# Kernel optimization log

Measured on AMD Instinct MI355X. Metric: run time of the kernel, lower is better.

Reference implementation:

```python
import jax, jax.numpy as jnp
import numpy as np

B, C, H, W = 8, 512, 128, 128
WS = 8

def _proj(x, w, b):
    # 1x1 conv == channel GEMM: (B,C,H,W) x (Cout,Cin) -> (B,Cout,H,W)
    return jnp.einsum('bchw,oc->bohw', x, w) + b[None, :, None, None]

def _split_windows(x):
    # (B,C,H,W) -> (B*nH*nW, ws*ws, C)
    b, c, h, w = x.shape
    x = x.reshape(b, c, h // WS, WS, w // WS, WS)
    x = x.transpose(0, 2, 4, 3, 5, 1)
    return x.reshape(-1, WS * WS, c)

def _merge_windows(x, b, c, h, w):
    # (B*nH*nW, ws*ws, C) -> (B,C,H,W)
    x = x.reshape(b, h // WS, w // WS, WS, WS, c)
    x = x.transpose(0, 5, 1, 3, 2, 4)
    return x.reshape(b, c, h, w)

def setup_inputs() -> dict:
    key = jax.random.key(0)
    ks = jax.random.split(key, 9)
    s = 1.0 / np.sqrt(C)
    return {
        'x': jax.random.normal(ks[0], (B, C, H, W), jnp.float32),
        'wq': jax.random.normal(ks[1], (C, C), jnp.float32) * s,
        'bq': jnp.zeros((C,), jnp.float32),
        'wk': jax.random.normal(ks[2], (C, C), jnp.float32) * s,
        'bk': jnp.zeros((C,), jnp.float32),
        'wv': jax.random.normal(ks[3], (C, C), jnp.float32) * s,
        'bv': jnp.zeros((C,), jnp.float32),
        'wo': jax.random.normal(ks[4], (C, C), jnp.float32) * s,
        'bo': jnp.zeros((C,), jnp.float32),
    }

def reference(x, wq, bq, wk, bk, wv, bv, wo, bo):
    b, c, h, w = x.shape
    q = _split_windows(_proj(x, wq, bq))  # (nWin, ws*ws, C)
    k = _split_windows(_proj(x, wk, bk))
    v = _split_windows(_proj(x, wv, bv))
    attn = jnp.einsum('nqc,nkc->nqk', q, k) / jnp.sqrt(jnp.asarray(c, x.dtype))
    attn = jax.nn.softmax(attn, axis=-1)
    out = jnp.einsum('nqk,nkc->nqc', attn, v)
    out = _merge_windows(out, b, c, h, w)
    return _proj(out, wo, bo)
```

## Files before the change

### kernel.cpp

```cpp
#include <hip/hip_runtime.h>

typedef __attribute__((ext_vector_type(8))) short bf16x8;
typedef __attribute__((ext_vector_type(4))) float f32x4;

#define MFMA16(a, b, c) __builtin_amdgcn_mfma_f32_16x16x32_bf16((a), (b), (c), 0, 0, 0)

__device__ __forceinline__ float b2f(unsigned short u) {
  unsigned int v = ((unsigned int)u) << 16;
  return __builtin_bit_cast(float, v);
}
__device__ __forceinline__ unsigned short f2b(float f) {
  unsigned int u = __builtin_bit_cast(unsigned int, f);
  u += 0x7fffu + ((u >> 16) & 1u);
  return (unsigned short)(u >> 16);
}
__device__ __forceinline__ void gload16(const void* g, void* l) {
  __builtin_amdgcn_global_load_lds(
      (const __attribute__((address_space(1))) unsigned int*)g,
      (__attribute__((address_space(3))) unsigned int*)l, 16, 0, 0);
}

__global__ __launch_bounds__(256) void k_wprep(
    const float* __restrict__ wq, const float* __restrict__ wk,
    const float* __restrict__ wv, const float* __restrict__ wo,
    unsigned short* __restrict__ outbase) {
  const int z = blockIdx.z;
  const int t = threadIdx.x;
  if (z == 3) {
    const int r0 = blockIdx.x << 6, s0 = blockIdx.y << 6;
    const int row = r0 + (t >> 2), col = s0 + (t & 3) * 16;
    const float* src = wo + (size_t)row * 512 + col;
    unsigned short* dst = outbase + 786432 + (size_t)row * 512 + col;
    unsigned short o[16];
#pragma unroll
    for (int i = 0; i < 4; ++i) {
      const float4 v = ((const float4*)src)[i];
      o[i * 4 + 0] = f2b(v.x); o[i * 4 + 1] = f2b(v.y);
      o[i * 4 + 2] = f2b(v.z); o[i * 4 + 3] = f2b(v.w);
    }
    *(uint4*)dst = *(const uint4*)&o[0];
    *(uint4*)(dst + 8) = *(const uint4*)&o[8];
    return;
  }
  __shared__ unsigned short tile[64][72];
  const float* in = (z == 0) ? wq : (z == 1) ? wk : wv;
  unsigned short* out = outbase + (size_t)z * 262144u;
  const int r0 = blockIdx.x << 6, s0 = blockIdx.y << 6;
  {
    const int sl = t >> 3, rl = (t & 7) << 3;
#pragma unroll
    for (int pass = 0; pass < 2; ++pass) {
      const int s = sl + pass * 32;
      const float* src = in + (size_t)(s0 + s) * 512 + r0 + rl;
      const float4 f0 = ((const float4*)src)[0];
      const float4 f1 = ((const float4*)src)[1];
      tile[rl + 0][s] = f2b(f0.x);
      tile[rl + 1][s] = f2b(f0.y);
      tile[rl + 2][s] = f2b(f0.z);
      tile[rl + 3][s] = f2b(f0.w);
      tile[rl + 4][s] = f2b(f1.x);
      tile[rl + 5][s] = f2b(f1.y);
      tile[rl + 6][s] = f2b(f1.z);
      tile[rl + 7][s] = f2b(f1.w);
    }
  }
  __syncthreads();
  {
    const int rl = t >> 3, sl = (t & 7) << 3;
#pragma unroll
    for (int pass = 0; pass < 2; ++pass) {
      const int r = rl + pass * 32;
      uint4 v = *(const uint4*)&tile[r][sl];
      *(uint4*)(out + (size_t)(r0 + r) * 512 + s0 + sl) = v;
    }
  }
}

__global__ __launch_bounds__(256) void k_bias(
    const float* __restrict__ wo, const float* __restrict__ bv,
    const float* __restrict__ bo, const float* __restrict__ wk,
    const float* __restrict__ bq, float* __restrict__ bvo,
    float* __restrict__ u) {
  const int bid = blockIdx.x;
  if (bid < 2) {
    const int o = bid * 256 + threadIdx.x;
    float acc = bo[o];
    const float* row = wo + (size_t)o * 512;
    for (int j = 0; j < 512; ++j) acc += row[j] * bv[j];
    bvo[o] = acc;
  } else {
    const int c = (bid - 2) * 256 + threadIdx.x;
    float acc = 0.f;
    for (int o = 0; o < 512; ++o) acc += bq[o] * wk[(size_t)o * 512 + c];
    u[c] = acc;
  }
}

__global__ __launch_bounds__(256, 2) void k_transpose(
    const float* __restrict__ X, unsigned short* __restrict__ XT,
    unsigned short* __restrict__ XV) {
  __shared__ float lds[2][16 * 512];
  const int hz = blockIdx.x;
  const int cg = blockIdx.y;
  const int b = blockIdx.z;
  const int h0 = hz << 2;
  const int c0 = cg << 7;
  const int t = threadIdx.x;
  const float* xb = X + (size_t)b * 8388608u + (size_t)c0 * 16384 +
                    (size_t)h0 * 128;

  auto stage = [&](int s) {
    float* dstb = lds[s & 1];
#pragma unroll
    for (int i = 0; i < 8; ++i) {
      const int cl = i * 2 + (t >> 7);
      const int q = (i * 256 + t) & 127;
      gload16(xb + (size_t)(s * 16 + cl) * 16384 + q * 4,
              dstb + (size_t)(i * 256 + t) * 4);
    }
  };

  auto consume = [&](int s) {
    const float* L = lds[s & 1];
#pragma unroll
    for (int pp = 0; pp < 2; ++pp) {
      const int p = t + pp * 256;
      unsigned short o[16];
#pragma unroll
      for (int cl = 0; cl < 16; ++cl) o[cl] = f2b(L[cl * 512 + p]);
      unsigned short* d =
          XT + ((size_t)b * 16384 + h0 * 128 + p) * 512 + c0 + s * 16;
      *(uint4*)d = *(const uint4*)&o[0];
      *(uint4*)(d + 8) = *(const uint4*)&o[8];
    }
    {
      const int cl = t >> 4, win = t & 15;
      unsigned short ov[32];
#pragma unroll
      for (int hr = 0; hr < 4; ++hr) {
        const float4 f0 = *(const float4*)&L[cl * 512 + hr * 128 + win * 8];
        const float4 f1 = *(const float4*)&L[cl * 512 + hr * 128 + win * 8 + 4];
        ov[hr * 8 + 0] = f2b(f0.x); ov[hr * 8 + 1] = f2b(f0.y);
        ov[hr * 8 + 2] = f2b(f0.z); ov[hr * 8 + 3] = f2b(f0.w);
        ov[hr * 8 + 4] = f2b(f1.x); ov[hr * 8 + 5] = f2b(f1.y);
        ov[hr * 8 + 6] = f2b(f1.z); ov[hr * 8 + 7] = f2b(f1.w);
      }
      const int wing = b * 256 + (h0 >> 3) * 16 + win;
      const int tok0 = (h0 & 4) * 8;
      unsigned short* dv = XV + (size_t)(c0 + s * 16 + cl) * 131072 +
                           (size_t)wing * 64 + tok0;
      *(uint4*)(dv + 0) = *(const uint4*)&ov[0];
      *(uint4*)(dv + 8) = *(const uint4*)&ov[8];
      *(uint4*)(dv + 16) = *(const uint4*)&ov[16];
      *(uint4*)(dv + 24) = *(const uint4*)&ov[24];
    }
  };

  stage(0);
#pragma unroll
  for (int s = 0; s < 8; ++s) {
    if (s < 7) {
      stage(s + 1);
      asm volatile("s_waitcnt vmcnt(8)" ::: "memory");
    } else {
      asm volatile("s_waitcnt vmcnt(0)" ::: "memory");
    }
    __builtin_amdgcn_s_barrier();
    consume(s);
    __builtin_amdgcn_s_barrier();
  }
}

template <int MODE>
__global__ __launch_bounds__(512, 2) void k_gemm256(
    const unsigned short* __restrict__ A, const unsigned short* __restrict__ B,
    const float* __restrict__ bias0, void* __restrict__ C0v) {
  __shared__ unsigned short lsA[4][256 * 32];
  __shared__ unsigned short lsB[4][256 * 32];
  const int bid = blockIdx.x;
  int mt, nt, sel = 0;
  if (MODE == 0) {
    const int work = ((bid & 7) << 7) + (bid >> 3);
    mt = work >> 1; nt = work & 1;
  } else if (MODE == 2) {
    const int work = ((bid & 7) << 7) + (bid >> 3);
    nt = work >> 1; mt = work & 1;
  } else {
    sel = bid >> 2;
    mt = bid & 1; nt = (bid >> 1) & 1;
  }
  const unsigned short* Ap = A;
  const unsigned short* Bp = B;
  if (MODE == 4) {
    Ap = sel ? A + 786432 : A + 262144;
    Bp = sel ? A + 524288 : A;
  }
  const int m0 = mt << 8, n0 = nt << 8;

  const int t = threadIdx.x;
  const int l = t & 63;
  const int lr = l & 15, lg = l >> 4;
  const int w = t >> 6;
  const int wr = w >> 2, wc = w & 3;
  const int ra = wr << 7, rb = wc << 6;
  const int srowS = t >> 2;
  const int scolS = (t & 3) << 3;
  const int ssw = ((srowS >> 1) & 3) << 3;
  const int scolX = scolS ^ ssw;
  const int rsw = (lr >> 1) & 3;
  const int rco = (lg ^ rsw) * 8;

  f32x4 acc[8][4];
#pragma unroll
  for (int i = 0; i < 8; ++i)
#pragma unroll
    for (int j = 0; j < 4; ++j) acc[i][j] = f32x4{0.f, 0.f, 0.f, 0.f};

  auto stage = [&](int kt) {
    const int buf = kt & 3, k0 = kt << 5;
#pragma unroll
    for (int hh = 0; hh < 2; ++hh) {
      gload16(Ap + (size_t)(m0 + srowS + hh * 128) * 512 + k0 + scolX,
              &lsA[buf][(srowS + hh * 128) * 32 + scolS]);
      gload16(Bp + (size_t)(n0 + srowS + hh * 128) * 512 + k0 + scolX,
              &lsB[buf][(srowS + hh * 128) * 32 + scolS]);
    }
  };
  auto compute = [&](int kt) {
    const int buf = kt & 3;
    bf16x8 af[8], bfv[4];
#pragma unroll
    for (int i = 0; i < 8; ++i)
      af[i] = *(const bf16x8*)&lsA[buf][(ra + i * 16 + lr) * 32 + rco];
#pragma unroll
    for (int j = 0; j < 4; ++j)
      bfv[j] = *(const bf16x8*)&lsB[buf][(rb + j * 16 + lr) * 32 + rco];
    __builtin_amdgcn_s_setprio(1);
#pragma unroll
    for (int i = 0; i < 8; ++i)
#pragma unroll
      for (int j = 0; j < 4; ++j)
        acc[i][j] = MFMA16(af[i], bfv[j], acc[i][j]);
    __builtin_amdgcn_s_setprio(0);
  };

  stage(0); stage(1); stage(2);

#define GITER(kt, vm)                                        \
  asm volatile("s_waitcnt vmcnt(" #vm ")" ::: "memory");     \
  __builtin_amdgcn_s_barrier();                              \
  __builtin_amdgcn_sched_barrier(0);                         \
  if ((kt) + 3 < 16) stage((kt) + 3);                        \
  compute(kt);                                               \
  __builtin_amdgcn_sched_barrier(0);                         \
  __builtin_amdgcn_s_barrier();

  GITER(0, 8)  GITER(1, 8)  GITER(2, 8)  GITER(3, 8)
  GITER(4, 8)  GITER(5, 8)  GITER(6, 8)  GITER(7, 8)
  GITER(8, 8)  GITER(9, 8)  GITER(10, 8) GITER(11, 8)
  GITER(12, 8) GITER(13, 8) GITER(14, 4) GITER(15, 0)
#undef GITER

#pragma unroll
  for (int i = 0; i < 8; ++i) {
    const int cmb = m0 + ra + i * 16 + lg * 4;
#pragma unroll
    for (int j = 0; j < 4; ++j) {
      const int cn = n0 + rb + j * 16 + lr;
      const float bn = (MODE == 0) ? bias0[cn] : 0.f;
#pragma unroll
      for (int r = 0; r < 4; ++r) {
        const int cm = cmb + r;
        if (MODE == 0) {
          ((unsigned short*)C0v)[(size_t)cm * 512 + cn] = f2b(acc[i][j][r] + bn);
        } else if (MODE == 2) {
          const float val = acc[i][j][r] + bias0[cm];
          const int bb = cn >> 14, p = cn & 16383;
          __builtin_nontemporal_store(
              val, (float*)C0v + (size_t)bb * 8388608 + (size_t)cm * 16384 + p);
        } else {
          unsigned short* Cs =
              (unsigned short*)C0v + (sel ? 1048576 : 1572864);
          Cs[(size_t)cm * 512 + cn] = f2b(acc[i][j][r]);
        }
      }
    }
  }
}

__global__ __launch_bounds__(256) void k_attn(
    const unsigned short* __restrict__ Q, const unsigned short* __restrict__ XT,
    const unsigned short* __restrict__ XV, unsigned short* __restrict__ Y) {
  __shared__ unsigned short P_lds[4][64][72];
  const int t = threadIdx.x, w = t >> 6, l = t & 63;
  const int lr = l & 15, lg = l >> 4;
  const int grp = ((blockIdx.x & 7) << 6) + (blockIdx.x >> 3);
  const int win = grp * 4 + w;
  const int b = win >> 8, th = (win >> 4) & 15, tw = win & 15;
  const size_t p_base = (size_t)b * 16384 + (size_t)th * 1024 + (size_t)tw * 8;
  const size_t rowpix = p_base + (size_t)(lr >> 3) * 128 + (lr & 7);
  const unsigned short* qbase = Q + rowpix * 512;
  const unsigned short* kbase = XT + rowpix * 512;

  f32x4 acc[4][4];
#pragma unroll
  for (int i = 0; i < 4; ++i)
#pragma unroll
    for (int j = 0; j < 4; ++j) acc[i][j] = f32x4{0.f, 0.f, 0.f, 0.f};

  bf16x8 kp[2][4], qp[2][4];
#pragma unroll
  for (int pp = 0; pp < 2; ++pp) {
    const int co = pp * 32 + lg * 8;
#pragma unroll
    for (int i = 0; i < 4; ++i) {
      kp[pp][i] = *(const bf16x8*)(kbase + (size_t)i * 131072 + co);
      qp[pp][i] = *(const bf16x8*)(qbase + (size_t)i * 131072 + co);
    }
  }
#pragma unroll
  for (int cs = 0; cs < 16; ++cs) {
    const int cb = cs & 1;
    __builtin_amdgcn_s_setprio(1);
#pragma unroll
    for (int mt = 0; mt < 4; ++mt)
#pragma unroll
      for (int qt = 0; qt < 4; ++qt)
        acc[mt][qt] = MFMA16(kp[cb][mt], qp[cb][qt], acc[mt][qt]);
    __builtin_amdgcn_s_setprio(0);
    if (cs + 2 < 16) {
      const int co = (cs + 2) * 32 + lg * 8;
#pragma unroll
      for (int i = 0; i < 4; ++i) {
        kp[cb][i] = *(const bf16x8*)(kbase + (size_t)i * 131072 + co);
        qp[cb][i] = *(const bf16x8*)(qbase + (size_t)i * 131072 + co);
      }
    }
  }

  const float scale = 0.044194173824159216f;
#pragma unroll
  for (int qt = 0; qt < 4; ++qt) {
    float pv[4][4];
    float mx = -3.0e38f;
#pragma unroll
    for (int mt = 0; mt < 4; ++mt)
#pragma unroll
      for (int j = 0; j < 4; ++j) {
        const float s = acc[mt][qt][j] * scale;
        pv[mt][j] = s;
        mx = fmaxf(mx, s);
      }
    mx = fmaxf(mx, __shfl_xor(mx, 16));
    mx = fmaxf(mx, __shfl_xor(mx, 32));
    float sum = 0.f;
#pragma unroll
    for (int mt = 0; mt < 4; ++mt)
#pragma unroll
      for (int j = 0; j < 4; ++j) {
        const float e = __expf(pv[mt][j] - mx);
        pv[mt][j] = e;
        sum += e;
      }
    sum += __shfl_xor(sum, 16);
    sum += __shfl_xor(sum, 32);
    const float inv = 1.f / sum;
#pragma unroll
    for (int mt = 0; mt < 4; ++mt)
#pragma unroll
      for (int j = 0; j < 4; j += 2) {
        const unsigned int pk =
            (unsigned int)f2b(pv[mt][j] * inv) |
            ((unsigned int)f2b(pv[mt][j + 1] * inv) << 16);
        *(unsigned int*)&P_lds[w][qt * 16 + lr][mt * 16 + lg * 4 + j] = pk;
      }
  }

  bf16x8 pa0[4], pa1[4];
#pragma unroll
  for (int qt = 0; qt < 4; ++qt) {
    pa0[qt] = *(const bf16x8*)&P_lds[w][qt * 16 + lr][lg * 8];
    pa1[qt] = *(const bf16x8*)&P_lds[w][qt * 16 + lr][32 + lg * 8];
  }
  const unsigned short* vbase =
      XV + (size_t)lr * 131072 + (size_t)win * 64 + lg * 8;
  unsigned short* ystore =
      Y + (p_base + (size_t)(lg >> 1) * 128 + ((lg & 1) << 2)) * 512 + lr;

  bf16x8 v0p[2], v1p[2];
#pragma unroll
  for (int pp = 0; pp < 2; ++pp) {
    const unsigned short* vp = vbase + (size_t)pp * (16 * 131072);
    v0p[pp] = *(const bf16x8*)vp;
    v1p[pp] = *(const bf16x8*)(vp + 32);
  }
#pragma unroll
  for (int nt = 0; nt < 32; ++nt) {
    const int cb = nt & 1;
    f32x4 o[4];
    __builtin_amdgcn_s_setprio(1);
#pragma unroll
    for (int qt = 0; qt < 4; ++qt) {
      o[qt] = f32x4{0.f, 0.f, 0.f, 0.f};
      o[qt] = MFMA16(pa0[qt], v0p[cb], o[qt]);
      o[qt] = MFMA16(pa1[qt], v1p[cb], o[qt]);
    }
    __builtin_amdgcn_s_setprio(0);
    if (nt + 2 < 32) {
      const unsigned short* vp = vbase + (size_t)(nt + 2) * (16 * 131072);
      v0p[cb] = *(const bf16x8*)vp;
      v1p[cb] = *(const bf16x8*)(vp + 32);
    }
#pragma unroll
    for (int qt = 0; qt < 4; ++qt)
#pragma unroll
      for (int r = 0; r < 4; ++r)
        ystore[(size_t)qt * 131072 + r * 512 + nt * 16] = f2b(o[qt][r]);
  }
}

extern "C" void kernel_launch(void* const* d_in, const int* in_sizes, int n_in,
                              void* d_out, int out_size, void* d_ws,
                              size_t ws_size, hipStream_t stream) {
  (void)in_sizes; (void)n_in; (void)out_size;
  const float* x = (const float*)d_in[0];
  const float* wq = (const float*)d_in[1];
  const float* bq = (const float*)d_in[2];
  const float* wk = (const float*)d_in[3];
  const float* bk = (const float*)d_in[4];
  const float* wv = (const float*)d_in[5];
  const float* bv = (const float*)d_in[6];
  const float* wo = (const float*)d_in[7];
  const float* bo = (const float*)d_in[8];
  (void)bk;

  const size_t NEED = (size_t)(2097152 + 3 * 67108864) * 2;
  if (ws_size < NEED) return;

  unsigned short* wb = (unsigned short*)d_ws;
  unsigned short* wvo = wb + 1048576;
  float* bvo = (float*)(wb + 1310720);
  float* ub = (float*)(wb + 1311744);
  unsigned short* Bqk = wb + 1572864;
  unsigned short* xT = wb + 2097152;
  unsigned short* xV = xT + 67108864;
  unsigned short* Ybuf = xV + 67108864;
  unsigned short* Tq = (unsigned short*)d_out;

  k_wprep<<<dim3(8, 8, 4), 256, 0, stream>>>(wq, wk, wv, wo, wb);
  k_bias<<<4, 256, 0, stream>>>(wo, bv, bo, wk, bq, bvo, ub);
  k_gemm256<4><<<8, 512, 0, stream>>>(wb, wb, nullptr, wb);
  k_transpose<<<dim3(32, 4, 8), 256, 0, stream>>>(x, xT, xV);
  k_gemm256<0><<<1024, 512, 0, stream>>>(xT, Bqk, ub, Tq);
  k_attn<<<512, 256, 0, stream>>>(Tq, xT, xV, Ybuf);
  k_gemm256<2><<<1024, 512, 0, stream>>>(wvo, Ybuf, bvo, d_out);
}
```

Baseline: 580.1 us.

## Retile transpose kernel into smaller channel blocks with padded LDS and buffered writes

The transpose/convert kernel now handles 32 channels per block instead of 128 and launches 4x more blocks. Its LDS shrinks and each row is padded to 516 floats to avoid bank conflicts, which lets 4 blocks run per CU. The XT row-major output is accumulated in registers across stages, so each token writes a full 64-byte chunk at the end instead of 32-byte pieces per stage. The XV writes are split so each thread emits 16-byte stores. The cost is more register pressure from the 64 buffered values and more blocks to schedule.

```diff
diff --git a/kernel.cpp b/kernel.cpp
--- a/kernel.cpp
+++ b/kernel.cpp
@@ -96,78 +96,78 @@
   }
 }
 
-__global__ __launch_bounds__(256, 2) void k_transpose(
+__global__ __launch_bounds__(256, 4) void k_transpose(
     const float* __restrict__ X, unsigned short* __restrict__ XT,
     unsigned short* __restrict__ XV) {
-  __shared__ float lds[2][16 * 512];
+  __shared__ float lds[2][8 * 516];
   const int hz = blockIdx.x;
-  const int cg = blockIdx.y;
+  const int cgB = blockIdx.y;
   const int b = blockIdx.z;
   const int h0 = hz << 2;
-  const int c0 = cg << 7;
+  const int c0 = cgB << 5;
   const int t = threadIdx.x;
-  const float* xb = X + (size_t)b * 8388608u + (size_t)c0 * 16384 +
-                    (size_t)h0 * 128;
+  const float* xb = X + (size_t)b * 8388608u + (size_t)h0 * 128;
 
   auto stage = [&](int s) {
     float* dstb = lds[s & 1];
 #pragma unroll
-    for (int i = 0; i < 8; ++i) {
-      const int cl = i * 2 + (t >> 7);
-      const int q = (i * 256 + t) & 127;
-      gload16(xb + (size_t)(s * 16 + cl) * 16384 + q * 4,
-              dstb + (size_t)(i * 256 + t) * 4);
+    for (int i = 0; i < 4; ++i) {
+      const int q4 = i * 256 + t;
+      const int cl = q4 >> 7;
+      const int q = q4 & 127;
+      gload16(xb + (size_t)(c0 + s * 8 + cl) * 16384 + q * 4,
+              dstb + (size_t)cl * 516 + q * 4);
     }
   };
 
-  auto consume = [&](int s) {
+  unsigned short xo[2][32];
+
+  stage(0);
+#pragma unroll
+  for (int s = 0; s < 4; ++s) {
+    if (s < 3) {
+      stage(s + 1);
+      asm volatile("s_waitcnt vmcnt(4)" ::: "memory");
+    } else {
+      asm volatile("s_waitcnt vmcnt(0)" ::: "memory");
+    }
+    __builtin_amdgcn_s_barrier();
     const float* L = lds[s & 1];
 #pragma unroll
     for (int pp = 0; pp < 2; ++pp) {
       const int p = t + pp * 256;
-      unsigned short o[16];
-#pragma unroll
-      for (int cl = 0; cl < 16; ++cl) o[cl] = f2b(L[cl * 512 + p]);
-      unsigned short* d =
-          XT + ((size_t)b * 16384 + h0 * 128 + p) * 512 + c0 + s * 16;
-      *(uint4*)d = *(const uint4*)&o[0];
-      *(uint4*)(d + 8) = *(const uint4*)&o[8];
+#pragma unroll
+      for (int cl = 0; cl < 8; ++cl)
+        xo[pp][s * 8 + cl] = f2b(L[cl * 516 + p]);
     }
     {
-      const int cl = t >> 4, win = t & 15;
-      unsigned short ov[32];
-#pragma unroll
-      for (int hr = 0; hr < 4; ++hr) {
-        const float4 f0 = *(const float4*)&L[cl * 512 + hr * 128 + win * 8];
-        const float4 f1 = *(const float4*)&L[cl * 512 + hr * 128 + win * 8 + 4];
-        ov[hr * 8 + 0] = f2b(f0.x); ov[hr * 8 + 1] = f2b(f0.y);
-        ov[hr * 8 + 2] = f2b(f0.z); ov[hr * 8 + 3] = f2b(f0.w);
-        ov[hr * 8 + 4] = f2b(f1.x); ov[hr * 8 + 5] = f2b(f1.y);
-        ov[hr * 8 + 6] = f2b(f1.z); ov[hr * 8 + 7] = f2b(f1.w);
-      }
+      const int cl = t >> 5, win = t & 15, hb = (t >> 4) & 1;
       const int wing = b * 256 + (h0 >> 3) * 16 + win;
       const int tok0 = (h0 & 4) * 8;
-      unsigned short* dv = XV + (size_t)(c0 + s * 16 + cl) * 131072 +
-                           (size_t)wing * 64 + tok0;
-      *(uint4*)(dv + 0) = *(const uint4*)&ov[0];
-      *(uint4*)(dv + 8) = *(const uint4*)&ov[8];
-      *(uint4*)(dv + 16) = *(const uint4*)&ov[16];
-      *(uint4*)(dv + 24) = *(const uint4*)&ov[24];
-    }
-  };
-
-  stage(0);
-#pragma unroll
-  for (int s = 0; s < 8; ++s) {
-    if (s < 7) {
-      stage(s + 1);
-      asm volatile("s_waitcnt vmcnt(8)" ::: "memory");
-    } else {
-      asm volatile("s_waitcnt vmcnt(0)" ::: "memory");
+      unsigned short* dvb =
+          XV + (size_t)(c0 + s * 8 + cl) * 131072 + (size_t)wing * 64 + tok0;
+#pragma unroll
+      for (int k = 0; k < 2; ++k) {
+        const int hr = hb + k * 2;
+        const float* src = &L[cl * 516 + hr * 128 + win * 8];
+        unsigned short ov[8];
+#pragma unroll
+        for (int j = 0; j < 8; ++j) ov[j] = f2b(src[j]);
+        *(uint4*)(dvb + hr * 8) = *(const uint4*)ov;
+      }
     }
     __builtin_amdgcn_s_barrier();
-    consume(s);
-    __builtin_amdgcn_s_barrier();
+  }
+
+#pragma unroll
+  for (int pp = 0; pp < 2; ++pp) {
+    const int p = t + pp * 256;
+    unsigned short* d =
+        XT + ((size_t)b * 16384 + (size_t)h0 * 128 + p) * 512 + c0;
+    *(uint4*)(d + 0) = *(const uint4*)&xo[pp][0];
+    *(uint4*)(d + 8) = *(const uint4*)&xo[pp][8];
+    *(uint4*)(d + 16) = *(const uint4*)&xo[pp][16];
+    *(uint4*)(d + 24) = *(const uint4*)&xo[pp][24];
   }
 }
 
@@ -450,7 +450,7 @@
   k_wprep<<<dim3(8, 8, 4), 256, 0, stream>>>(wq, wk, wv, wo, wb);
   k_bias<<<4, 256, 0, stream>>>(wo, bv, bo, wk, bq, bvo, ub);
   k_gemm256<4><<<8, 512, 0, stream>>>(wb, wb, nullptr, wb);
-  k_transpose<<<dim3(32, 4, 8), 256, 0, stream>>>(x, xT, xV);
+  k_transpose<<<dim3(32, 16, 8), 256, 0, stream>>>(x, xT, xV);
   k_gemm256<0><<<1024, 512, 0, stream>>>(xT, Bqk, ub, Tq);
   k_attn<<<512, 256, 0, stream>>>(Tq, xT, xV, Ybuf);
   k_gemm256<2><<<1024, 512, 0, stream>>>(wvo, Ybuf, bvo, d_out);
```

After: 521.0 us (median of 2 runs). 10.2% less time.
